# Optimization experiments

Hardware: AMD Instinct MI355X
Metric: run time of the kernel (lower is better)

Reference implementation:

```python
import jax, jax.numpy as jnp
import numpy as np

BLOCK = 32          # MXFP block size (OCP microscaling)
EMAX_FP4 = 2.0      # max exponent of FP4 E2M1 (max value 6.0 = 1.5 * 2^2)
FP4_MAX = 6.0       # saturation value of E2M1
E8M0_MIN, E8M0_MAX = -127.0, 127.0


def _quant_dequant_mxfp(t, block_dim):
    """Fake-quantize tensor t to MXFP4 (E2M1 elements, shared E8M0 scale per
    block of 32 along block_dim), then dequantize back to float."""
    t = jnp.moveaxis(t, block_dim, -1)
    shape = t.shape
    nb = shape[-1] // BLOCK
    tb = t.reshape(shape[:-1] + (nb, BLOCK))

    # shared power-of-two scale from block absmax: scale = 2^(floor(log2 amax) - emax)
    amax = jnp.max(jnp.abs(tb), axis=-1, keepdims=True)
    safe_amax = jnp.where(amax > 0, amax, 1.0)
    shared_exp = jnp.floor(jnp.log2(safe_amax)) - EMAX_FP4
    scale = jnp.exp2(jnp.clip(shared_exp, E8M0_MIN, E8M0_MAX))

    v = tb / scale
    sign = jnp.sign(v)
    a = jnp.clip(jnp.abs(v), 0.0, FP4_MAX)  # saturate to E2M1 max
    # E2M1 quantization step: 0.5 for |v|<2 (incl. subnormals), 1 for [2,4), 2 for [4,6]
    e = jnp.clip(jnp.floor(jnp.log2(jnp.maximum(a, 2.0 ** -10))), 0.0, EMAX_FP4)
    step = jnp.exp2(e - 1.0)
    q = jnp.round(a / step) * step

    deq = (sign * q * scale).reshape(shape)
    return jnp.moveaxis(deq, -1, block_dim)


def setup_inputs() -> dict:
    key = jax.random.key(0)
    kx, kw, kb = jax.random.split(key, 3)
    x = jax.random.normal(kx, (64, 4096), dtype=jnp.float32)
    weight = jax.random.normal(kw, (11008, 4096), dtype=jnp.float32) * 0.02
    bias = jax.random.normal(kb, (11008,), dtype=jnp.float32) * 0.02
    return {"x": x, "weight": weight, "bias": bias}


def reference(x, weight, bias):
    # layer_type = 'XqWqBq': MXFP4 quant-dequant on x (last dim), w (in_features
    # dim, block_dim=1) and b (dim 0), fused with the linear GEMM.
    x_dq = _quant_dequant_mxfp(x, block_dim=-1)        # [T, Din]
    w_dq = _quant_dequant_mxfp(weight, block_dim=1)    # [Dout, Din]
    b_dq = _quant_dequant_mxfp(bias, block_dim=0)      # [Dout]
    return jnp.einsum('ti,oi->to', x_dq, w_dq) + b_dq  # [T, Dout]
```

## Files before the change

kernel.cpp:

```cpp
#include <hip/hip_runtime.h>
#include <hip/hip_bf16.h>

#define DIN    4096
#define DOUT   11008
#define TM     64
#define KSPLIT 8
#define KCHUNK (DIN / KSPLIT)
#define NCHUNKS (DOUT / 16)

typedef __attribute__((ext_vector_type(8))) short  bf16x8;
typedef __attribute__((ext_vector_type(4))) float  f32x4;

__device__ inline void mx_block_scale(float amax, float& scale, float& inv_scale) {
    float safe = amax > 0.0f ? amax : 1.0f;
    int e  = (int)((__float_as_uint(safe) >> 23) & 255) - 127;
    int se = e - 2;
    if (se < -127) se = -127;
    scale     = ldexpf(1.0f, se);
    inv_scale = ldexpf(1.0f, -se);
}

__device__ inline float mx_qd(float v, float scale, float inv_scale) {
    float a = fabsf(v) * inv_scale;
    a = fminf(a, 6.0f);
    float step  = (a < 2.0f) ? 0.5f : (a < 4.0f) ? 1.0f : 2.0f;
    float rstep = (a < 2.0f) ? 2.0f : (a < 4.0f) ? 1.0f : 0.5f;
    float q = rintf(a * rstep) * step;
    return copysignf(q * scale, v);
}

__device__ inline short bf16_trunc(float f) {
    return (short)(__float_as_uint(f) >> 16);
}

__global__ __launch_bounds__(256) void quant_x_kernel(const float* __restrict__ x,
                                                      unsigned short* __restrict__ x_dq) {
    int gid = blockIdx.x * 256 + threadIdx.x;
    const float4 v = *(const float4*)(x + (size_t)gid * 4);
    float am = fmaxf(fmaxf(fabsf(v.x), fabsf(v.y)), fmaxf(fabsf(v.z), fabsf(v.w)));
    am = fmaxf(am, __shfl_xor(am, 1));
    am = fmaxf(am, __shfl_xor(am, 2));
    am = fmaxf(am, __shfl_xor(am, 4));
    float scale, inv;
    mx_block_scale(am, scale, inv);
    ushort4 q;
    q.x = (unsigned short)bf16_trunc(mx_qd(v.x, scale, inv));
    q.y = (unsigned short)bf16_trunc(mx_qd(v.y, scale, inv));
    q.z = (unsigned short)bf16_trunc(mx_qd(v.z, scale, inv));
    q.w = (unsigned short)bf16_trunc(mx_qd(v.w, scale, inv));
    *(ushort4*)(x_dq + (size_t)gid * 4) = q;
}

__global__ __launch_bounds__(256) void gemm_kernel(const unsigned short* __restrict__ x_dq,
                                                   const float* __restrict__ wgt,
                                                   float* __restrict__ partial) {
    const int lane  = threadIdx.x & 63;
    const int wid   = threadIdx.x >> 6;
    const int w     = blockIdx.x * 4 + wid;
    const int nch   = w % NCHUNKS;
    const int split = w / NCHUNKS;
    const int nlo   = lane & 15;
    const int kq    = lane >> 4;
    const int kbase = split * KCHUNK + kq * 8;

    const float*          wp = wgt  + (size_t)(nch * 16 + nlo) * DIN + kbase;
    const unsigned short* xp = x_dq + (size_t)nlo * DIN + kbase;

    f32x4 acc0 = {0.f,0.f,0.f,0.f};
    f32x4 acc1 = {0.f,0.f,0.f,0.f};
    f32x4 acc2 = {0.f,0.f,0.f,0.f};
    f32x4 acc3 = {0.f,0.f,0.f,0.f};

    float4 w0 = *(const float4*)(wp);
    float4 w1 = *(const float4*)(wp + 4);

    for (int kk = 0; kk < KCHUNK; kk += 32) {
        float4 c0 = w0, c1 = w1;
        if (kk + 32 < KCHUNK) {
            w0 = *(const float4*)(wp + kk + 32);
            w1 = *(const float4*)(wp + kk + 36);
        }
        bf16x8 a0 = *(const bf16x8*)(xp + kk);
        bf16x8 a1 = *(const bf16x8*)(xp + 16 * DIN + kk);
        bf16x8 a2 = *(const bf16x8*)(xp + 32 * DIN + kk);
        bf16x8 a3 = *(const bf16x8*)(xp + 48 * DIN + kk);

        float am = fmaxf(fmaxf(fmaxf(fabsf(c0.x), fabsf(c0.y)), fmaxf(fabsf(c0.z), fabsf(c0.w))),
                         fmaxf(fmaxf(fabsf(c1.x), fabsf(c1.y)), fmaxf(fabsf(c1.z), fabsf(c1.w))));
        am = fmaxf(am, __shfl_xor(am, 16));
        am = fmaxf(am, __shfl_xor(am, 32));
        float scale, inv;
        mx_block_scale(am, scale, inv);

        bf16x8 bf;
        bf[0] = bf16_trunc(mx_qd(c0.x, scale, inv));
        bf[1] = bf16_trunc(mx_qd(c0.y, scale, inv));
        bf[2] = bf16_trunc(mx_qd(c0.z, scale, inv));
        bf[3] = bf16_trunc(mx_qd(c0.w, scale, inv));
        bf[4] = bf16_trunc(mx_qd(c1.x, scale, inv));
        bf[5] = bf16_trunc(mx_qd(c1.y, scale, inv));
        bf[6] = bf16_trunc(mx_qd(c1.z, scale, inv));
        bf[7] = bf16_trunc(mx_qd(c1.w, scale, inv));

        acc0 = __builtin_amdgcn_mfma_f32_16x16x32_bf16(a0, bf, acc0, 0, 0, 0);
        acc1 = __builtin_amdgcn_mfma_f32_16x16x32_bf16(a1, bf, acc1, 0, 0, 0);
        acc2 = __builtin_amdgcn_mfma_f32_16x16x32_bf16(a2, bf, acc2, 0, 0, 0);
        acc3 = __builtin_amdgcn_mfma_f32_16x16x32_bf16(a3, bf, acc3, 0, 0, 0);
    }

    float* pp = partial + (size_t)split * (TM * DOUT) + (size_t)(nch * 16 + nlo);
    const int mrow = kq * 4;
    #pragma unroll
    for (int r = 0; r < 4; ++r) {
        pp[(size_t)(mrow + r) * DOUT]      = acc0[r];
        pp[(size_t)(16 + mrow + r) * DOUT] = acc1[r];
        pp[(size_t)(32 + mrow + r) * DOUT] = acc2[r];
        pp[(size_t)(48 + mrow + r) * DOUT] = acc3[r];
    }
}

__global__ __launch_bounds__(256) void reduce_bias_kernel(const float* __restrict__ partial,
                                                          const float* __restrict__ bias,
                                                          float* __restrict__ out) {
    int gid = blockIdx.x * 256 + threadIdx.x;
    float s = 0.f;
    #pragma unroll
    for (int i = 0; i < KSPLIT; ++i)
        s += partial[(size_t)i * (TM * DOUT) + gid];
    int n = gid % DOUT;
    float v = bias[n];
    float am = fabsf(v);
    am = fmaxf(am, __shfl_xor(am, 1));
    am = fmaxf(am, __shfl_xor(am, 2));
    am = fmaxf(am, __shfl_xor(am, 4));
    am = fmaxf(am, __shfl_xor(am, 8));
    am = fmaxf(am, __shfl_xor(am, 16));
    float scale, inv;
    mx_block_scale(am, scale, inv);
    out[gid] = s + mx_qd(v, scale, inv);
}

extern "C" void kernel_launch(void* const* d_in, const int* in_sizes, int n_in,
                              void* d_out, int out_size, void* d_ws, size_t ws_size,
                              hipStream_t stream) {
    const float* x    = (const float*)d_in[0];
    const float* wgt  = (const float*)d_in[1];
    const float* bias = (const float*)d_in[2];
    float* out = (float*)d_out;

    unsigned short* x_dq    = (unsigned short*)d_ws;
    float*          partial = (float*)((char*)d_ws + 512 * 1024);

    quant_x_kernel<<<256, 256, 0, stream>>>(x, x_dq);
    gemm_kernel<<<NCHUNKS * KSPLIT / 4, 256, 0, stream>>>(x_dq, wgt, partial);
    reduce_bias_kernel<<<TM * DOUT / 256, 256, 0, stream>>>(partial, bias, out);
}
```

Before: 290.5 us.

## Deepen weight prefetch to two stages and halve K-split

Weight loads are now prefetched two iterations ahead, and each next block's scale is computed after the MFMAs so the shuffles overlap with matrix work. The loop is unrolled by 4. KSPLIT drops from 8 to 4, which halves the partial-sum traffic written by the GEMM and read back by the reduce kernel, but it also halves the number of wavefronts and doubles the loop length per wave. Register pressure goes up with the extra in-flight buffers, and the clamped tail prefetch issues a few redundant loads.

```diff
diff --git a/kernel.cpp b/kernel.cpp
--- a/kernel.cpp
+++ b/kernel.cpp
@@ -4,7 +4,7 @@
 #define DIN    4096
 #define DOUT   11008
 #define TM     64
-#define KSPLIT 8
+#define KSPLIT 4
 #define KCHUNK (DIN / KSPLIT)
 #define NCHUNKS (DOUT / 16)
 
@@ -31,6 +31,11 @@
 
 __device__ inline short bf16_trunc(float f) {
     return (short)(__float_as_uint(f) >> 16);
+}
+
+__device__ inline float blk_absmax8(const float4& a, const float4& b) {
+    return fmaxf(fmaxf(fmaxf(fabsf(a.x), fabsf(a.y)), fmaxf(fabsf(a.z), fabsf(a.w))),
+                 fmaxf(fmaxf(fabsf(b.x), fabsf(b.y)), fmaxf(fabsf(b.z), fabsf(b.w))));
 }
 
 __global__ __launch_bounds__(256) void quant_x_kernel(const float* __restrict__ x,
@@ -71,41 +76,49 @@
     f32x4 acc2 = {0.f,0.f,0.f,0.f};
     f32x4 acc3 = {0.f,0.f,0.f,0.f};
 
-    float4 w0 = *(const float4*)(wp);
-    float4 w1 = *(const float4*)(wp + 4);
+    float4 wa0 = *(const float4*)(wp);
+    float4 wa1 = *(const float4*)(wp + 4);
+    float4 wb0 = *(const float4*)(wp + 32);
+    float4 wb1 = *(const float4*)(wp + 36);
+    float am = blk_absmax8(wa0, wa1);
+    am = fmaxf(am, __shfl_xor(am, 16));
+    am = fmaxf(am, __shfl_xor(am, 32));
+    float scale, inv;
+    mx_block_scale(am, scale, inv);
 
+    #pragma unroll 4
     for (int kk = 0; kk < KCHUNK; kk += 32) {
-        float4 c0 = w0, c1 = w1;
-        if (kk + 32 < KCHUNK) {
-            w0 = *(const float4*)(wp + kk + 32);
-            w1 = *(const float4*)(wp + kk + 36);
-        }
+        const int kpre = (kk + 64 < KCHUNK) ? kk + 64 : KCHUNK - 32;
+        float4 wc0 = *(const float4*)(wp + kpre);
+        float4 wc1 = *(const float4*)(wp + kpre + 4);
+
         bf16x8 a0 = *(const bf16x8*)(xp + kk);
         bf16x8 a1 = *(const bf16x8*)(xp + 16 * DIN + kk);
         bf16x8 a2 = *(const bf16x8*)(xp + 32 * DIN + kk);
         bf16x8 a3 = *(const bf16x8*)(xp + 48 * DIN + kk);
 
-        float am = fmaxf(fmaxf(fmaxf(fabsf(c0.x), fabsf(c0.y)), fmaxf(fabsf(c0.z), fabsf(c0.w))),
-                         fmaxf(fmaxf(fabsf(c1.x), fabsf(c1.y)), fmaxf(fabsf(c1.z), fabsf(c1.w))));
-        am = fmaxf(am, __shfl_xor(am, 16));
-        am = fmaxf(am, __shfl_xor(am, 32));
-        float scale, inv;
-        mx_block_scale(am, scale, inv);
-
         bf16x8 bf;
-        bf[0] = bf16_trunc(mx_qd(c0.x, scale, inv));
-        bf[1] = bf16_trunc(mx_qd(c0.y, scale, inv));
-        bf[2] = bf16_trunc(mx_qd(c0.z, scale, inv));
-        bf[3] = bf16_trunc(mx_qd(c0.w, scale, inv));
-        bf[4] = bf16_trunc(mx_qd(c1.x, scale, inv));
-        bf[5] = bf16_trunc(mx_qd(c1.y, scale, inv));
-        bf[6] = bf16_trunc(mx_qd(c1.z, scale, inv));
-        bf[7] = bf16_trunc(mx_qd(c1.w, scale, inv));
+        bf[0] = bf16_trunc(mx_qd(wa0.x, scale, inv));
+        bf[1] = bf16_trunc(mx_qd(wa0.y, scale, inv));
+        bf[2] = bf16_trunc(mx_qd(wa0.z, scale, inv));
+        bf[3] = bf16_trunc(mx_qd(wa0.w, scale, inv));
+        bf[4] = bf16_trunc(mx_qd(wa1.x, scale, inv));
+        bf[5] = bf16_trunc(mx_qd(wa1.y, scale, inv));
+        bf[6] = bf16_trunc(mx_qd(wa1.z, scale, inv));
+        bf[7] = bf16_trunc(mx_qd(wa1.w, scale, inv));
 
         acc0 = __builtin_amdgcn_mfma_f32_16x16x32_bf16(a0, bf, acc0, 0, 0, 0);
         acc1 = __builtin_amdgcn_mfma_f32_16x16x32_bf16(a1, bf, acc1, 0, 0, 0);
         acc2 = __builtin_amdgcn_mfma_f32_16x16x32_bf16(a2, bf, acc2, 0, 0, 0);
         acc3 = __builtin_amdgcn_mfma_f32_16x16x32_bf16(a3, bf, acc3, 0, 0, 0);
+
+        float amn = blk_absmax8(wb0, wb1);
+        amn = fmaxf(amn, __shfl_xor(amn, 16));
+        amn = fmaxf(amn, __shfl_xor(amn, 32));
+        mx_block_scale(amn, scale, inv);
+
+        wa0 = wb0; wa1 = wb1;
+        wb0 = wc0; wb1 = wc1;
     }
 
     float* pp = partial + (size_t)split * (TM * DOUT) + (size_t)(nch * 16 + nlo);
```

After: 274.4 us. 1.06x faster.
